# Optimization experiments

Hardware: AMD Instinct MI355X
Metric: run time of the kernel (lower is better)

The kernel has to match this reference:

```python
import jax, jax.numpy as jnp
import numpy as np

K = 5          # kernel_size
SIGMA = 1.5    # gaussian sigma
BETA = 0.3     # blend_beta


def setup_inputs() -> dict:
    key = jax.random.key(0)
    k1, k2, k3 = jax.random.split(key, 3)
    B, H, W = 4, 512, 512
    fire_map = jax.random.uniform(k1, (B, 1, H, W), dtype=jnp.float32)
    wind_u = jax.random.normal(k2, (B, 1, H, W), dtype=jnp.float32)
    wind_v = jax.random.normal(k3, (B, 1, H, W), dtype=jnp.float32)
    return {"fire_map": fire_map, "wind_u": wind_u, "wind_v": wind_v}


def reference(fire_map, wind_u, wind_v):
    B, C, H, W = fire_map.shape
    pad = K // 2
    # ---- spatially-varying direction kernel: [B, K, K, H, W] ----
    ax = jnp.arange(K, dtype=fire_map.dtype) - pad
    xx, yy = jnp.meshgrid(ax, ax, indexing='ij')           # [K, K]
    theta = jnp.arctan2(wind_v, wind_u + 1e-8)[:, 0]       # [B, H, W]
    cos_t = jnp.cos(theta)
    sin_t = jnp.sin(theta)
    proj = (xx[None, :, :, None, None] * cos_t[:, None, None, :, :]
            + yy[None, :, :, None, None] * sin_t[:, None, None, :, :])  # [B,K,K,H,W]
    weight = jnp.exp(-proj ** 2 / (2.0 * SIGMA ** 2))
    weight = weight / (weight.sum(axis=(1, 2), keepdims=True) + 1e-8)
    # ---- unfold with ZERO padding (F.unfold semantics) ----
    fp = jnp.pad(fire_map[:, 0], ((0, 0), (pad, pad), (pad, pad)))  # [B, H+2p, W+2p]
    patches = jnp.stack(
        [fp[:, i:i + H, j:j + W] for i in range(K) for j in range(K)], axis=1
    ).reshape(B, K, K, H, W)
    # ---- weighted sum + residual blend + clamp ----
    spread = (patches * weight).sum(axis=(1, 2))[:, None]  # [B, 1, H, W]
    spread = (1.0 - BETA) * spread + BETA * fire_map
    return jnp.clip(spread, 0.0, 1.0)
```

## Files before the change

### kernel.cpp

```cpp
#include <hip/hip_runtime.h>


constexpr int Wd = 512;
constexpr int Hd = 512;
constexpr int PW = 520;

__global__ __launch_bounds__(256, 4) void dirconv_kernel(
    const float* __restrict__ fire,
    const float* __restrict__ wu,
    const float* __restrict__ wv,
    float* __restrict__ out)
{
    constexpr float C1 = -0.3205988979753274f;
    constexpr float C2 = -0.6411977959506548f;
    constexpr float KB = 0.8007374029168082f;

    __shared__ float lds[6][PW];

    const int blk = blockIdx.x;
    const int b  = blk >> 8;
    const int y0 = (blk & 255) << 1;
    const int t  = threadIdx.x;
    const float* img = fire + (b << 18);

    const int lrow = t >> 7;
    const int x = (t & 127) << 2;
    const int p = (b << 18) + ((y0 + lrow) << 9) + x;

    float4 u4 = *reinterpret_cast<const float4*>(wu + p);
    float4 v4 = *reinterpret_cast<const float4*>(wv + p);

    if (t < 12) {
        int r = t >> 1, sd = t & 1;
        *reinterpret_cast<float4*>(&lds[r][sd ? 516 : 0]) =
            make_float4(0.f, 0.f, 0.f, 0.f);
    }
#pragma unroll
    for (int j = 0; j < 3; ++j) {
        int id = t + (j << 8);
        int r  = id >> 7;
        int q  = id & 127;
        int gr = y0 - 2 + r;
        float4 val = make_float4(0.f, 0.f, 0.f, 0.f);
        if ((unsigned)gr < (unsigned)Hd)
            val = *reinterpret_cast<const float4*>(img + (gr << 9) + (q << 2));
        *reinterpret_cast<float4*>(&lds[r][4 + (q << 2)]) = val;
    }

    float ua[4] = {u4.x, u4.y, u4.z, u4.w};
    float va[4] = {v4.x, v4.y, v4.z, v4.w};

    float A1[4], A4[4], B1a[4], B4a[4], WsA[4], S[4];
    float c1[4], c2[4], c3[4], c4[4], d1[4], d2[4], d3[4], d4[4];

#pragma unroll
    for (int k = 0; k < 4; ++k) {
        float un = ua[k] + 1e-8f;
        float vv = va[k];
        float r2 = fmaf(un, un, vv * vv);
        r2 = fmaxf(r2, 1e-36f);
        float ir = __builtin_amdgcn_rsqf(r2);
        float c = un * ir;
        float s = vv * ir;
        float a1 = exp2f(c * c * C1);
        float g  = exp2f(c * s * C2);
        float b1 = KB * __builtin_amdgcn_rcpf(a1);
        float a2 = a1 * a1;  float A4v = a2 * a2;
        float b2 = b1 * b1;  float B4v = b2 * b2;
        float gi  = __builtin_amdgcn_rcpf(g);
        float g2 = g * g,   gi2 = gi * gi;
        float g4 = g2 * g2, gi4 = gi2 * gi2;
        c1[k] = b1 * g;  c2[k] = b1 * gi;  c3[k] = B4v * g2;  c4[k] = B4v * gi2;
        d1[k] = b1 * g2; d2[k] = b1 * gi2; d3[k] = B4v * g4;  d4[k] = B4v * gi4;
        A1[k] = a1; A4[k] = A4v; B1a[k] = b1; B4a[k] = B4v;
        float sc = 1.0f + ((c1[k] + c2[k]) + (c3[k] + c4[k]));
        float sd = 1.0f + ((d1[k] + d2[k]) + (d3[k] + d4[k]));
        float base = fmaf(2.0f, b1 + B4v, 1.0f);
        WsA[k] = fmaf(2.0f, fmaf(a1, sc, A4v * sd), base);
        S[k] = 0.0f;
    }

    __syncthreads();

    float4 fcen = make_float4(0.f, 0.f, 0.f, 0.f);
#pragma unroll
    for (int di = 0; di < 5; ++di) {
        const int ai = di - 2;
        const int r = lrow + di;
        float4 L = *reinterpret_cast<const float4*>(&lds[r][x]);
        float4 M = *reinterpret_cast<const float4*>(&lds[r][x + 4]);
        float4 R4v = *reinterpret_cast<const float4*>(&lds[r][x + 8]);
        if (di == 2) fcen = M;
        float fv[8] = {L.z, L.w, M.x, M.y, M.z, M.w, R4v.x, R4v.y};
#pragma unroll
        for (int k = 0; k < 4; ++k) {
            float fm2 = fv[k], fm1 = fv[k + 1], f0 = fv[k + 2];
            float fp1 = fv[k + 3], fp2 = fv[k + 4];
            if (ai == 0) {
                float R = fmaf(B4a[k], fm2 + fp2, fmaf(B1a[k], fm1 + fp1, f0));
                S[k] += R;
            } else if (ai == 1) {
                float R = fmaf(c4[k], fm2, fmaf(c2[k], fm1,
                          fmaf(c1[k], fp1, fmaf(c3[k], fp2, f0))));
                S[k] = fmaf(A1[k], R, S[k]);
            } else if (ai == -1) {
                float R = fmaf(c3[k], fm2, fmaf(c1[k], fm1,
                          fmaf(c2[k], fp1, fmaf(c4[k], fp2, f0))));
                S[k] = fmaf(A1[k], R, S[k]);
            } else if (ai == 2) {
                float R = fmaf(d4[k], fm2, fmaf(d2[k], fm1,
                          fmaf(d1[k], fp1, fmaf(d3[k], fp2, f0))));
                S[k] = fmaf(A4[k], R, S[k]);
            } else {
                float R = fmaf(d3[k], fm2, fmaf(d1[k], fm1,
                          fmaf(d2[k], fp1, fmaf(d4[k], fp2, f0))));
                S[k] = fmaf(A4[k], R, S[k]);
            }
        }
    }

    float fcena[4] = {fcen.x, fcen.y, fcen.z, fcen.w};
    float4 o;
#pragma unroll
    for (int k = 0; k < 4; ++k) {
        float inv = __builtin_amdgcn_rcpf(WsA[k] + 1e-8f);
        float sp = S[k] * inv;
        float r = fmaf(0.7f, sp, 0.3f * fcena[k]);
        r = fminf(fmaxf(r, 0.0f), 1.0f);
        (&o.x)[k] = r;
    }
    *reinterpret_cast<float4*>(out + p) = o;
}

extern "C" void kernel_launch(void* const* d_in, const int* in_sizes, int n_in,
                              void* d_out, int out_size, void* d_ws, size_t ws_size,
                              hipStream_t stream) {
    const float* fire = (const float*)d_in[0];
    const float* wu   = (const float*)d_in[1];
    const float* wv   = (const float*)d_in[2];
    float* out        = (float*)d_out;
    int blocks = out_size >> 10;
    dirconv_kernel<<<blocks, 256, 0, stream>>>(fire, wu, wv, out);
}
```

Measured before the change: 10.07 us.

## Process one output row per block with two pixels per thread

Each block now produces a single output row instead of two, and each thread handles two pixels instead of four. The grid doubles, the LDS tile shrinks to five rows, and launch bounds are raised to allow more resident blocks. The aim is more parallelism and occupancy with fewer registers per thread. In exchange, halo reuse drops, since each block loads five input rows for one output row instead of six for two, and LDS and global loads move to float2 width.

```diff
diff --git a/kernel.cpp b/kernel.cpp
--- a/kernel.cpp
+++ b/kernel.cpp
@@ -5,7 +5,7 @@
 constexpr int Hd = 512;
 constexpr int PW = 520;
 
-__global__ __launch_bounds__(256, 4) void dirconv_kernel(
+__global__ __launch_bounds__(256, 8) void dirconv_kernel(
     const float* __restrict__ fire,
     const float* __restrict__ wu,
     const float* __restrict__ wv,
@@ -15,22 +15,21 @@
     constexpr float C2 = -0.6411977959506548f;
     constexpr float KB = 0.8007374029168082f;
 
-    __shared__ float lds[6][PW];
+    __shared__ float lds[5][PW];
 
     const int blk = blockIdx.x;
-    const int b  = blk >> 8;
-    const int y0 = (blk & 255) << 1;
-    const int t  = threadIdx.x;
+    const int b   = blk >> 9;
+    const int y0  = blk & 511;
+    const int t   = threadIdx.x;
     const float* img = fire + (b << 18);
 
-    const int lrow = t >> 7;
-    const int x = (t & 127) << 2;
-    const int p = (b << 18) + ((y0 + lrow) << 9) + x;
+    const int x = t << 1;
+    const int p = (b << 18) + (y0 << 9) + x;
 
-    float4 u4 = *reinterpret_cast<const float4*>(wu + p);
-    float4 v4 = *reinterpret_cast<const float4*>(wv + p);
+    float2 u2 = *reinterpret_cast<const float2*>(wu + p);
+    float2 v2 = *reinterpret_cast<const float2*>(wv + p);
 
-    if (t < 12) {
+    if (t < 10) {
         int r = t >> 1, sd = t & 1;
         *reinterpret_cast<float4*>(&lds[r][sd ? 516 : 0]) =
             make_float4(0.f, 0.f, 0.f, 0.f);
@@ -38,23 +37,25 @@
 #pragma unroll
     for (int j = 0; j < 3; ++j) {
         int id = t + (j << 8);
-        int r  = id >> 7;
-        int q  = id & 127;
-        int gr = y0 - 2 + r;
-        float4 val = make_float4(0.f, 0.f, 0.f, 0.f);
-        if ((unsigned)gr < (unsigned)Hd)
-            val = *reinterpret_cast<const float4*>(img + (gr << 9) + (q << 2));
-        *reinterpret_cast<float4*>(&lds[r][4 + (q << 2)]) = val;
+        if (id < 640) {
+            int r  = id >> 7;
+            int q  = id & 127;
+            int gr = y0 - 2 + r;
+            float4 val = make_float4(0.f, 0.f, 0.f, 0.f);
+            if ((unsigned)gr < (unsigned)Hd)
+                val = *reinterpret_cast<const float4*>(img + (gr << 9) + (q << 2));
+            *reinterpret_cast<float4*>(&lds[r][4 + (q << 2)]) = val;
+        }
     }
 
-    float ua[4] = {u4.x, u4.y, u4.z, u4.w};
-    float va[4] = {v4.x, v4.y, v4.z, v4.w};
+    float ua[2] = {u2.x, u2.y};
+    float va[2] = {v2.x, v2.y};
 
-    float A1[4], A4[4], B1a[4], B4a[4], WsA[4], S[4];
-    float c1[4], c2[4], c3[4], c4[4], d1[4], d2[4], d3[4], d4[4];
+    float A1[2], A4[2], B1a[2], B4a[2], WsA[2], S[2];
+    float c1[2], c2[2], c3[2], c4[2], d1[2], d2[2], d3[2], d4[2];
 
 #pragma unroll
-    for (int k = 0; k < 4; ++k) {
+    for (int k = 0; k < 2; ++k) {
         float un = ua[k] + 1e-8f;
         float vv = va[k];
         float r2 = fmaf(un, un, vv * vv);
@@ -82,18 +83,17 @@
 
     __syncthreads();
 
-    float4 fcen = make_float4(0.f, 0.f, 0.f, 0.f);
+    float fc0 = 0.f, fc1 = 0.f;
 #pragma unroll
     for (int di = 0; di < 5; ++di) {
         const int ai = di - 2;
-        const int r = lrow + di;
-        float4 L = *reinterpret_cast<const float4*>(&lds[r][x]);
-        float4 M = *reinterpret_cast<const float4*>(&lds[r][x + 4]);
-        float4 R4v = *reinterpret_cast<const float4*>(&lds[r][x + 8]);
-        if (di == 2) fcen = M;
-        float fv[8] = {L.z, L.w, M.x, M.y, M.z, M.w, R4v.x, R4v.y};
+        float2 a = *reinterpret_cast<const float2*>(&lds[di][x + 2]);
+        float2 m = *reinterpret_cast<const float2*>(&lds[di][x + 4]);
+        float2 r2v = *reinterpret_cast<const float2*>(&lds[di][x + 6]);
+        if (di == 2) { fc0 = m.x; fc1 = m.y; }
+        float fv[6] = {a.x, a.y, m.x, m.y, r2v.x, r2v.y};
 #pragma unroll
-        for (int k = 0; k < 4; ++k) {
+        for (int k = 0; k < 2; ++k) {
             float fm2 = fv[k], fm1 = fv[k + 1], f0 = fv[k + 2];
             float fp1 = fv[k + 3], fp2 = fv[k + 4];
             if (ai == 0) {
@@ -119,17 +119,17 @@
         }
     }
 
-    float fcena[4] = {fcen.x, fcen.y, fcen.z, fcen.w};
-    float4 o;
+    float2 o;
+    float fca[2] = {fc0, fc1};
 #pragma unroll
-    for (int k = 0; k < 4; ++k) {
+    for (int k = 0; k < 2; ++k) {
         float inv = __builtin_amdgcn_rcpf(WsA[k] + 1e-8f);
         float sp = S[k] * inv;
-        float r = fmaf(0.7f, sp, 0.3f * fcena[k]);
+        float r = fmaf(0.7f, sp, 0.3f * fca[k]);
         r = fminf(fmaxf(r, 0.0f), 1.0f);
         (&o.x)[k] = r;
     }
-    *reinterpret_cast<float4*>(out + p) = o;
+    *reinterpret_cast<float2*>(out + p) = o;
 }
 
 extern "C" void kernel_launch(void* const* d_in, const int* in_sizes, int n_in,
@@ -139,6 +139,6 @@
     const float* wu   = (const float*)d_in[1];
     const float* wv   = (const float*)d_in[2];
     float* out        = (float*)d_out;
-    int blocks = out_size >> 10;
+    int blocks = out_size >> 9;
     dirconv_kernel<<<blocks, 256, 0, stream>>>(fire, wu, wv, out);
 }
```

Result: no change. 10.22 us (+1.5%).
